# Kernel tuning notes

Measured on AMD Instinct MI355X. Metric: run time of the kernel, lower is better.

## Reference

```python
import jax, jax.numpy as jnp
import numpy as np

N, E, F_IN = 50000, 250000, 128
H1, H2, HEADS = 64, 32, 4
D1 = H1 * HEADS   # 256 = conv1 output dim (concat)
D2 = H2 * HEADS   # 128 = conv2 output dim (concat)
EPS_BN = 1e-5


def setup_inputs() -> dict:
    key = jax.random.key(0)
    ks = iter(jax.random.split(key, 64))
    def nrm(shape, scale=0.05):
        return jax.random.normal(next(ks), shape, dtype=jnp.float32) * scale
    inp = {}
    inp['x'] = jax.random.normal(next(ks), (N, F_IN), dtype=jnp.float32)
    inp['edge_index'] = jax.random.randint(next(ks), (2, E), 0, N, dtype=jnp.int32)
    inp['neg_edge_index'] = jax.random.randint(next(ks), (2, E), 0, N, dtype=jnp.int32)
    # conv1: TransformerConv(F_IN, 64, heads=4, beta=True, concat=True)
    inp['Wq1'] = nrm((F_IN, D1)); inp['bq1'] = jnp.zeros((D1,), jnp.float32)
    inp['Wk1'] = nrm((F_IN, D1)); inp['bk1'] = jnp.zeros((D1,), jnp.float32)
    inp['Wv1'] = nrm((F_IN, D1)); inp['bv1'] = jnp.zeros((D1,), jnp.float32)
    inp['Ws1'] = nrm((F_IN, D1)); inp['bs1'] = jnp.zeros((D1,), jnp.float32)
    inp['Wb1'] = nrm((3 * D1, 1))
    inp['g1'] = jnp.ones((D1,), jnp.float32); inp['be1'] = jnp.zeros((D1,), jnp.float32)
    inp['m1'] = nrm((D1,), 0.01); inp['v1'] = jax.random.uniform(next(ks), (D1,), dtype=jnp.float32) + 0.5
    # conv2: TransformerConv(256, 32, heads=4, beta=True, concat=True)
    inp['Wq2'] = nrm((D1, D2)); inp['bq2'] = jnp.zeros((D2,), jnp.float32)
    inp['Wk2'] = nrm((D1, D2)); inp['bk2'] = jnp.zeros((D2,), jnp.float32)
    inp['Wv2'] = nrm((D1, D2)); inp['bv2'] = jnp.zeros((D2,), jnp.float32)
    inp['Ws2'] = nrm((D1, D2)); inp['bs2'] = jnp.zeros((D2,), jnp.float32)
    inp['Wb2'] = nrm((3 * D2, 1))
    inp['g2'] = jnp.ones((D2,), jnp.float32); inp['be2'] = jnp.zeros((D2,), jnp.float32)
    inp['m2'] = nrm((D2,), 0.01); inp['v2'] = jax.random.uniform(next(ks), (D2,), dtype=jnp.float32) + 0.5
    # conv3: TransformerConv(128, 1, heads=1, beta=True, concat=False)
    inp['Wq3'] = nrm((D2, 1)); inp['bq3'] = jnp.zeros((1,), jnp.float32)
    inp['Wk3'] = nrm((D2, 1)); inp['bk3'] = jnp.zeros((1,), jnp.float32)
    inp['Wv3'] = nrm((D2, 1)); inp['bv3'] = jnp.zeros((1,), jnp.float32)
    inp['Ws3'] = nrm((D2, 1)); inp['bs3'] = jnp.zeros((1,), jnp.float32)
    inp['Wb3'] = nrm((3, 1))
    inp['c1'] = jnp.float32(0.5); inp['c2'] = jnp.float32(0.5)
    return inp


def _tconv(h, src, dst, Wq, bq, Wk, bk, Wv, bv, Ws, bs, Wb, heads, dh):
    # PyG TransformerConv with beta=True, root_weight=True. Messages flow src -> dst.
    n = h.shape[0]
    q = (h @ Wq + bq).reshape(n, heads, dh)
    k = (h @ Wk + bk).reshape(n, heads, dh)
    v = (h @ Wv + bv).reshape(n, heads, dh)
    score = jnp.einsum('ehd,ehd->eh', q[dst], k[src]) / jnp.sqrt(jnp.float32(dh))  # [E,H]
    m = jax.ops.segment_max(score, dst, num_segments=n)
    m = jnp.where(jnp.isfinite(m), m, jnp.float32(0.0))  # empty segments
    p = jnp.exp(score - m[dst])
    denom = jax.ops.segment_sum(p, dst, num_segments=n)
    alpha = p / (denom[dst] + 1e-16)
    out = jax.ops.segment_sum(alpha[:, :, None] * v[src], dst, num_segments=n)  # [N,H,dh]
    out = out.reshape(n, heads * dh)  # concat (heads=1 for conv3 -> same as mean)
    x_r = h @ Ws + bs
    beta = jax.nn.sigmoid(jnp.concatenate([out, x_r, out - x_r], axis=-1) @ Wb)  # [N,1]
    return beta * x_r + (1.0 - beta) * out


def _bn_eval(x, g, b, m, v):
    return (x - m) * jax.lax.rsqrt(v + EPS_BN) * g + b


def reference(x, edge_index, neg_edge_index,
              Wq1, bq1, Wk1, bk1, Wv1, bv1, Ws1, bs1, Wb1, g1, be1, m1, v1,
              Wq2, bq2, Wk2, bk2, Wv2, bv2, Ws2, bs2, Wb2, g2, be2, m2, v2,
              Wq3, bq3, Wk3, bk3, Wv3, bv3, Ws3, bs3, Wb3, c1, c2):
    src, dst = edge_index[0], edge_index[1]
    h = _tconv(x, src, dst, Wq1, bq1, Wk1, bk1, Wv1, bv1, Ws1, bs1, Wb1, HEADS, H1)
    h = jax.nn.elu(_bn_eval(h, g1, be1, m1, v1))
    h = _tconv(h, src, dst, Wq2, bq2, Wk2, bk2, Wv2, bv2, Ws2, bs2, Wb2, HEADS, H2)
    z = jax.nn.elu(_bn_eval(h, g2, be2, m2, v2))
    pos = -jnp.log(jax.nn.sigmoid(jnp.sum(z[src] * z[dst], axis=1)) + 1e-15).mean()
    ns, nd = neg_edge_index[0], neg_edge_index[1]
    neg = -jnp.log(1.0 - jax.nn.sigmoid(jnp.sum(z[ns] * z[nd], axis=1)) + 1e-15).mean()
    r_loss = pos + neg
    x_out = _tconv(z, src, dst, Wq3, bq3, Wk3, bk3, Wv3, bv3, Ws3, bs3, Wb3, 1, 1)
    return (x_out, r_loss, c1, c2)
```

## Files before the change

kernel.cpp:

```cpp
#include <hip/hip_runtime.h>
#include <hip/hip_bf16.h>

template<int BM, int BN, int BK>
__global__ __launch_bounds__(256) void sgemm_bias(
    const float* __restrict__ A, const float* __restrict__ W,
    const float* __restrict__ bias, float* __restrict__ C,
    int Nr, int K, int Dout)
{
  __shared__ float As[BK][BM];
  __shared__ float Ws[BK][BN];
  const int t  = threadIdx.x;
  const int tx = t & 15;
  const int ty = t >> 4;
  const int row0 = blockIdx.x * BM;
  const int col0 = blockIdx.y * BN;
  float acc[4][4] = {};
  for (int kb = 0; kb < K; kb += BK) {
    {
      int m  = t >> 2;
      int kq = (t & 3) * 8;
      int r  = row0 + m;
      float4 a0, a1;
      if (r < Nr) {
        const float* p = A + (long long)r * K + kb + kq;
        a0 = *(const float4*)p;
        a1 = *(const float4*)(p + 4);
      } else {
        a0 = make_float4(0.f,0.f,0.f,0.f); a1 = a0;
      }
      As[kq+0][m]=a0.x; As[kq+1][m]=a0.y; As[kq+2][m]=a0.z; As[kq+3][m]=a0.w;
      As[kq+4][m]=a1.x; As[kq+5][m]=a1.y; As[kq+6][m]=a1.z; As[kq+7][m]=a1.w;
    }
    {
      int cw = tx * 4;
#pragma unroll
      for (int it = 0; it < 2; ++it) {
        int kw = ty + it * 16;
        float4 w4 = *(const float4*)(W + (long long)(kb + kw) * Dout + col0 + cw);
        *(float4*)&Ws[kw][cw] = w4;
      }
    }
    __syncthreads();
#pragma unroll
    for (int kk = 0; kk < BK; ++kk) {
      float4 a4 = *(const float4*)&As[kk][ty * 4];
      float4 b4 = *(const float4*)&Ws[kk][tx * 4];
      float av[4] = {a4.x, a4.y, a4.z, a4.w};
      float bv[4] = {b4.x, b4.y, b4.z, b4.w};
#pragma unroll
      for (int i = 0; i < 4; ++i)
#pragma unroll
        for (int j = 0; j < 4; ++j)
          acc[i][j] += av[i] * bv[j];
    }
    __syncthreads();
  }
  float4 bb = *(const float4*)(bias + col0 + tx * 4);
  float bv4[4] = {bb.x, bb.y, bb.z, bb.w};
#pragma unroll
  for (int i = 0; i < 4; ++i) {
    int r = row0 + ty * 4 + i;
    if (r < Nr) {
      float4 o;
      o.x = acc[i][0] + bv4[0];
      o.y = acc[i][1] + bv4[1];
      o.z = acc[i][2] + bv4[2];
      o.w = acc[i][3] + bv4[3];
      *(float4*)(C + (long long)r * Dout + col0 + tx * 4) = o;
    }
  }
}

__global__ __launch_bounds__(256) void csr_hist(
    const int* __restrict__ ei, int E, int* __restrict__ cnt)
{
  int e = blockIdx.x * 256 + threadIdx.x;
  if (e >= E) return;
  atomicAdd(&cnt[ei[E + e]], 1);
}

__global__ __launch_bounds__(256) void csr_scan1(
    const int* __restrict__ cnt, int* __restrict__ excl,
    int* __restrict__ chunkSums, int N)
{
  int b = blockIdx.x, t = threadIdx.x;
  int lane = t & 63, w = t >> 6;
  int base = b * 1024 + t * 4;
  int c[4];
#pragma unroll
  for (int j = 0; j < 4; ++j) c[j] = (base + j < N) ? cnt[base + j] : 0;
  int ts = c[0] + c[1] + c[2] + c[3];
  int s = ts;
#pragma unroll
  for (int d = 1; d < 64; d <<= 1) {
    int u = __shfl_up(s, d, 64);
    if (lane >= d) s += u;
  }
  __shared__ int wsum[4];
  if (lane == 63) wsum[w] = s;
  __syncthreads();
  int woff = 0;
  for (int i = 0; i < w; ++i) woff += wsum[i];
  int off = woff + s - ts;
#pragma unroll
  for (int j = 0; j < 4; ++j) {
    if (base + j < N) excl[base + j] = off;
    off += c[j];
  }
  if (t == 0) chunkSums[b] = wsum[0] + wsum[1] + wsum[2] + wsum[3];
}

__global__ void csr_scan2(int* __restrict__ chunkSums, int nch,
                          int* __restrict__ rowptr, int N, int E)
{
  int lane = threadIdx.x;
  int v = (lane < nch) ? chunkSums[lane] : 0;
  int s = v;
#pragma unroll
  for (int d = 1; d < 64; d <<= 1) {
    int u = __shfl_up(s, d, 64);
    if (lane >= d) s += u;
  }
  if (lane < nch) chunkSums[lane] = s - v;
  if (lane == 0) rowptr[N] = E;
}

__global__ __launch_bounds__(256) void csr_scan3(
    int* __restrict__ rowptr, const int* __restrict__ chunkSums, int N)
{
  int i = blockIdx.x * 256 + threadIdx.x;
  if (i < N) rowptr[i] += chunkSums[i >> 10];
}

__global__ __launch_bounds__(256) void csr_scatter(
    const int* __restrict__ ei, int E, const int* __restrict__ rowptr,
    int* __restrict__ fill, int* __restrict__ csr_src)
{
  int e = blockIdx.x * 256 + threadIdx.x;
  if (e >= E) return;
  int s = ei[e], d = ei[E + e];
  int pos = atomicAdd(&fill[d], 1);
  csr_src[rowptr[d] + pos] = s;
}

template<int D, int H>
__global__ __launch_bounds__(256) void attn_fused(
    const int* __restrict__ rowptr, const int* __restrict__ csr_src,
    const float* __restrict__ q, const float* __restrict__ k,
    const float* __restrict__ v, float* __restrict__ o, int N)
{
  constexpr int PER = D / 64;
  constexpr int DH  = D / H;
  int node = blockIdx.x * 4 + (threadIdx.x >> 6);
  if (node >= N) return;
  int lane = threadIdx.x & 63;
  int j0   = lane * PER;
  const float inv = 1.0f / sqrtf((float)DH);

  float qv[PER];
  if constexpr (PER == 4) {
    float4 t4 = *(const float4*)(q + (long long)node * D + j0);
    qv[0]=t4.x; qv[1]=t4.y; qv[2]=t4.z; qv[3]=t4.w;
  } else {
    float2 t2 = *(const float2*)(q + (long long)node * D + j0);
    qv[0]=t2.x; qv[1]=t2.y;
  }

  float m = -INFINITY, den = 0.f;
  float acc[PER] = {};
  int beg = rowptr[node], end = rowptr[node + 1];
  for (int i = beg; i < end; ++i) {
    int s = csr_src[i];
    float kv[PER], vv[PER];
    if constexpr (PER == 4) {
      float4 t4 = *(const float4*)(k + (long long)s * D + j0);
      kv[0]=t4.x; kv[1]=t4.y; kv[2]=t4.z; kv[3]=t4.w;
      float4 u4 = *(const float4*)(v + (long long)s * D + j0);
      vv[0]=u4.x; vv[1]=u4.y; vv[2]=u4.z; vv[3]=u4.w;
    } else {
      float2 t2 = *(const float2*)(k + (long long)s * D + j0);
      kv[0]=t2.x; kv[1]=t2.y;
      float2 u2 = *(const float2*)(v + (long long)s * D + j0);
      vv[0]=u2.x; vv[1]=u2.y;
    }
    float dot = 0.f;
#pragma unroll
    for (int j = 0; j < PER; ++j) dot += qv[j] * kv[j];
    dot += __shfl_xor(dot, 8, 64);
    dot += __shfl_xor(dot, 4, 64);
    dot += __shfl_xor(dot, 2, 64);
    dot += __shfl_xor(dot, 1, 64);
    float score = dot * inv;
    float nm = fmaxf(m, score);
    float scale = __expf(m - nm);
    float p = __expf(score - nm);
    den = den * scale + p;
#pragma unroll
    for (int j = 0; j < PER; ++j) acc[j] = acc[j] * scale + p * vv[j];
    m = nm;
  }
  float r = 1.f / (den + 1e-16f);
  if constexpr (PER == 4) {
    float4 w4; w4.x = acc[0]*r; w4.y = acc[1]*r; w4.z = acc[2]*r; w4.w = acc[3]*r;
    *(float4*)(o + (long long)node * D + j0) = w4;
  } else {
    float2 w2; w2.x = acc[0]*r; w2.y = acc[1]*r;
    *(float2*)(o + (long long)node * D + j0) = w2;
  }
}

template<int D>
__global__ __launch_bounds__(256) void node_gate2(
    const float* __restrict__ o, const float* __restrict__ xr,
    const float* __restrict__ Wb, const float* __restrict__ g,
    const float* __restrict__ be, const float* __restrict__ bm,
    const float* __restrict__ bv, float* __restrict__ out, int N)
{
  constexpr int PER = D / 64;
  int node = blockIdx.x * 4 + (threadIdx.x >> 6);
  if (node >= N) return;
  int lane = threadIdx.x & 63;
  int j0   = lane * PER;
  float ov[PER], xv[PER];
  if constexpr (PER == 4) {
    float4 o4 = *(const float4*)(o  + (long long)node * D + j0);
    float4 x4 = *(const float4*)(xr + (long long)node * D + j0);
    ov[0]=o4.x; ov[1]=o4.y; ov[2]=o4.z; ov[3]=o4.w;
    xv[0]=x4.x; xv[1]=x4.y; xv[2]=x4.z; xv[3]=x4.w;
  } else {
    float2 o2 = *(const float2*)(o  + (long long)node * D + j0);
    float2 x2 = *(const float2*)(xr + (long long)node * D + j0);
    ov[0]=o2.x; ov[1]=o2.y;
    xv[0]=x2.x; xv[1]=x2.y;
  }
  float dot = 0.f;
#pragma unroll
  for (int i = 0; i < PER; ++i) {
    int j = j0 + i;
    dot += ov[i] * Wb[j] + xv[i] * Wb[D + j] + (ov[i] - xv[i]) * Wb[2 * D + j];
  }
#pragma unroll
  for (int off = 32; off >= 1; off >>= 1) dot += __shfl_xor(dot, off, 64);
  float beta = 1.f / (1.f + expf(-dot));
  float res[PER];
#pragma unroll
  for (int i = 0; i < PER; ++i) {
    int j = j0 + i;
    float h = beta * xv[i] + (1.f - beta) * ov[i];
    float y = (h - bm[j]) * rsqrtf(bv[j] + 1e-5f) * g[j] + be[j];
    res[i] = y > 0.f ? y : expf(y) - 1.f;
  }
  if constexpr (PER == 4) {
    float4 w; w.x=res[0]; w.y=res[1]; w.z=res[2]; w.w=res[3];
    *(float4*)(out + (long long)node * D + j0) = w;
  } else {
    float2 w; w.x=res[0]; w.y=res[1];
    *(float2*)(out + (long long)node * D + j0) = w;
  }
}

__global__ __launch_bounds__(256) void loss_kernel(
    const int* __restrict__ ei, const int* __restrict__ nei,
    const float* __restrict__ z, int E, float* __restrict__ acc)
{
  int lane = threadIdx.x & 63;
  int wib  = threadIdx.x >> 6;
  int sub  = lane >> 5, r = lane & 31;
  long long gw = ((long long)blockIdx.x * blockDim.x + threadIdx.x) >> 6;
  long long nw = ((long long)gridDim.x * blockDim.x) >> 6;
  float lpos = 0.f, lneg = 0.f;
  for (long long w = gw * 2 + sub; w < 2LL * E; w += nw * 2) {
    int isneg = (w >= E);
    const int* ep = isneg ? nei : ei;
    long long idx = isneg ? w - E : w;
    int s = ep[idx], d = ep[E + idx];
    float4 a = *(const float4*)(z + (long long)s * 128 + r * 4);
    float4 b = *(const float4*)(z + (long long)d * 128 + r * 4);
    float dot = a.x * b.x + a.y * b.y + a.z * b.z + a.w * b.w;
#pragma unroll
    for (int off = 16; off >= 1; off >>= 1) dot += __shfl_xor(dot, off, 64);
    if (r == 0) {
      float sg = 1.f / (1.f + expf(-dot));
      if (isneg) lneg += -logf(1.f - sg + 1e-15f);
      else       lpos += -logf(sg + 1e-15f);
    }
  }
#pragma unroll
  for (int off = 32; off >= 1; off >>= 1) {
    lpos += __shfl_xor(lpos, off, 64);
    lneg += __shfl_xor(lneg, off, 64);
  }
  __shared__ float sp[4], sn[4];
  if (lane == 0) { sp[wib] = lpos; sn[wib] = lneg; }
  __syncthreads();
  if (threadIdx.x == 0) {
    float P = 0.f, Ng = 0.f;
    for (int i = 0; i < 4; ++i) { P += sp[i]; Ng += sn[i]; }
    atomicAdd(acc, P);
    atomicAdd(acc + 1, Ng);
  }
}

__global__ __launch_bounds__(256) void gemv4(
    const float* __restrict__ z,
    const float* __restrict__ Wq, const float* __restrict__ bq,
    const float* __restrict__ Wk, const float* __restrict__ bk,
    const float* __restrict__ Wv, const float* __restrict__ bv,
    const float* __restrict__ Ws, const float* __restrict__ bs,
    float* __restrict__ q3, float* __restrict__ k3,
    float* __restrict__ v3, float* __restrict__ s3, int N)
{
  int node = blockIdx.x * 4 + (threadIdx.x >> 6);
  if (node >= N) return;
  int lane = threadIdx.x & 63;
  float2 zv = *(const float2*)(z + (long long)node * 128 + lane * 2);
  float aq = zv.x * Wq[lane*2] + zv.y * Wq[lane*2+1];
  float ak = zv.x * Wk[lane*2] + zv.y * Wk[lane*2+1];
  float av = zv.x * Wv[lane*2] + zv.y * Wv[lane*2+1];
  float as_ = zv.x * Ws[lane*2] + zv.y * Ws[lane*2+1];
#pragma unroll
  for (int off = 32; off >= 1; off >>= 1) {
    aq  += __shfl_xor(aq,  off, 64);
    ak  += __shfl_xor(ak,  off, 64);
    av  += __shfl_xor(av,  off, 64);
    as_ += __shfl_xor(as_, off, 64);
  }
  if (lane == 0) {
    q3[node] = aq + bq[0];
    k3[node] = ak + bk[0];
    v3[node] = av + bv[0];
    s3[node] = as_ + bs[0];
  }
}

__global__ __launch_bounds__(256) void attn3_node(
    const int* __restrict__ rowptr, const int* __restrict__ csr_src,
    const float* __restrict__ q3, const float* __restrict__ k3,
    const float* __restrict__ v3, const float* __restrict__ s3,
    const float* __restrict__ Wb3, float* __restrict__ out, int N)
{
  int n = blockIdx.x * 256 + threadIdx.x;
  if (n >= N) return;
  float qd = q3[n];
  float m = -INFINITY, den = 0.f, acc = 0.f;
  int beg = rowptr[n], end = rowptr[n + 1];
  for (int i = beg; i < end; ++i) {
    int s = csr_src[i];
    float sc = qd * k3[s];
    float nm = fmaxf(m, sc);
    float scale = __expf(m - nm);
    float p = __expf(sc - nm);
    den = den * scale + p;
    acc = acc * scale + p * v3[s];
    m = nm;
  }
  float on = acc / (den + 1e-16f);
  float xr = s3[n];
  float tv = on * Wb3[0] + xr * Wb3[1] + (on - xr) * Wb3[2];
  float b = 1.f / (1.f + expf(-tv));
  out[n] = b * xr + (1.f - b) * on;
}

__global__ void finalize_kernel(const float* __restrict__ acc,
                                const float* __restrict__ c1, const float* __restrict__ c2,
                                float* __restrict__ out, int N, int E)
{
  out[N]     = acc[0] / (float)E + acc[1] / (float)E;
  out[N + 1] = c1[0];
  out[N + 2] = c2[0];
}

extern "C" void kernel_launch(void* const* d_in, const int* in_sizes, int n_in,
                              void* d_out, int out_size, void* d_ws, size_t ws_size,
                              hipStream_t stream)
{
  const float* x   = (const float*)d_in[0];
  const int*   ei  = (const int*)d_in[1];
  const int*   nei = (const int*)d_in[2];
  const float* Wq1 = (const float*)d_in[3];  const float* bq1 = (const float*)d_in[4];
  const float* Wk1 = (const float*)d_in[5];  const float* bk1 = (const float*)d_in[6];
  const float* Wv1 = (const float*)d_in[7];  const float* bv1 = (const float*)d_in[8];
  const float* Ws1 = (const float*)d_in[9];  const float* bs1 = (const float*)d_in[10];
  const float* Wb1 = (const float*)d_in[11];
  const float* g1  = (const float*)d_in[12]; const float* be1 = (const float*)d_in[13];
  const float* m1  = (const float*)d_in[14]; const float* v1  = (const float*)d_in[15];
  const float* Wq2 = (const float*)d_in[16]; const float* bq2 = (const float*)d_in[17];
  const float* Wk2 = (const float*)d_in[18]; const float* bk2 = (const float*)d_in[19];
  const float* Wv2 = (const float*)d_in[20]; const float* bv2 = (const float*)d_in[21];
  const float* Ws2 = (const float*)d_in[22]; const float* bs2 = (const float*)d_in[23];
  const float* Wb2 = (const float*)d_in[24];
  const float* g2  = (const float*)d_in[25]; const float* be2 = (const float*)d_in[26];
  const float* m2  = (const float*)d_in[27]; const float* v2  = (const float*)d_in[28];
  const float* Wq3 = (const float*)d_in[29]; const float* bq3 = (const float*)d_in[30];
  const float* Wk3 = (const float*)d_in[31]; const float* bk3 = (const float*)d_in[32];
  const float* Wv3 = (const float*)d_in[33]; const float* bv3 = (const float*)d_in[34];
  const float* Ws3 = (const float*)d_in[35]; const float* bs3 = (const float*)d_in[36];
  const float* Wb3 = (const float*)d_in[37];
  const float* c1  = (const float*)d_in[38]; const float* c2  = (const float*)d_in[39];

  const int N = in_sizes[0] / 128;
  const int E = in_sizes[1] / 2;

  float* ws = (float*)d_ws;
  float* B0 = ws;
  float* B1 = B0 + (size_t)N * 256;
  float* B2 = B1 + (size_t)N * 256;
  int* rowptr = (int*)(B2 + (size_t)N * 256);
  int* cnt    = rowptr + (N + 1);
  int* csrs   = cnt + N;
  int* chks   = csrs + E;
  float* accbuf = (float*)(chks + 64);

  size_t need = ((size_t)3 * N * 256) * 4 + ((size_t)2 * N + 1 + E + 64) * 4 + 8;
  if (ws_size < need) return;

  float* out = (float*)d_out;
  dim3 blk(256);
  dim3 gemm1g((N + 63) / 64, 256 / 64);
  dim3 gemm2g((N + 63) / 64, 128 / 64);
  int ng  = (N + 3) / 4;
  int egE = (E + 255) / 256;
  int egN = (N + 255) / 256;
  int nch = (N + 1023) / 1024;

  (void)hipMemsetAsync(cnt, 0, (size_t)N * sizeof(int), stream);
  csr_hist<<<egE, blk, 0, stream>>>(ei, E, cnt);
  csr_scan1<<<nch, blk, 0, stream>>>(cnt, rowptr, chks, N);
  csr_scan2<<<1, 64, 0, stream>>>(chks, nch, rowptr, N, E);
  csr_scan3<<<egN, blk, 0, stream>>>(rowptr, chks, N);
  (void)hipMemsetAsync(cnt, 0, (size_t)N * sizeof(int), stream);
  csr_scatter<<<egE, blk, 0, stream>>>(ei, E, rowptr, cnt, csrs);

  sgemm_bias<64,64,32><<<gemm1g, blk, 0, stream>>>(x, Wq1, bq1, B0, N, 128, 256);
  sgemm_bias<64,64,32><<<gemm1g, blk, 0, stream>>>(x, Wk1, bk1, B1, N, 128, 256);
  sgemm_bias<64,64,32><<<gemm1g, blk, 0, stream>>>(x, Wv1, bv1, B2, N, 128, 256);
  attn_fused<256,4><<<ng, blk, 0, stream>>>(rowptr, csrs, B0, B1, B2, B0, N);
  sgemm_bias<64,64,32><<<gemm1g, blk, 0, stream>>>(x, Ws1, bs1, B1, N, 128, 256);
  node_gate2<256><<<ng, blk, 0, stream>>>(B0, B1, Wb1, g1, be1, m1, v1, B2, N);

  float* q2p = B0;
  float* k2p = B0 + (size_t)N * 128;
  float* v2p = B1;
  float* s2p = B1 + (size_t)N * 128;
  sgemm_bias<64,64,32><<<gemm2g, blk, 0, stream>>>(B2, Wq2, bq2, q2p, N, 256, 128);
  sgemm_bias<64,64,32><<<gemm2g, blk, 0, stream>>>(B2, Wk2, bk2, k2p, N, 256, 128);
  sgemm_bias<64,64,32><<<gemm2g, blk, 0, stream>>>(B2, Wv2, bv2, v2p, N, 256, 128);
  attn_fused<128,4><<<ng, blk, 0, stream>>>(rowptr, csrs, q2p, k2p, v2p, q2p, N);
  sgemm_bias<64,64,32><<<gemm2g, blk, 0, stream>>>(B2, Ws2, bs2, s2p, N, 256, 128);
  float* z = k2p;
  node_gate2<128><<<ng, blk, 0, stream>>>(q2p, s2p, Wb2, g2, be2, m2, v2, z, N);

  (void)hipMemsetAsync(accbuf, 0, 2 * sizeof(float), stream);
  loss_kernel<<<1024, blk, 0, stream>>>(ei, nei, z, E, accbuf);

  float* q3 = B1;
  float* k3 = B1 + (size_t)N;
  float* v3 = B1 + (size_t)2 * N;
  float* s3 = B1 + (size_t)3 * N;
  gemv4<<<ng, blk, 0, stream>>>(z, Wq3, bq3, Wk3, bk3, Wv3, bv3, Ws3, bs3, q3, k3, v3, s3, N);
  attn3_node<<<egN, blk, 0, stream>>>(rowptr, csrs, q3, k3, v3, s3, Wb3, out, N);

  finalize_kernel<<<1, 1, 0, stream>>>(accbuf, c1, c2, out, N, E);
}
```

Measured before the change: 893.4 us.

## Replace FP32 SIMT GEMMs with FP16 MFMA GEMMs using pretransposed weights

Swaps the shared-memory FP32 tiled SGEMM for a wavefront-level MFMA 16x16x32 f16 kernel. Activations are converted to half in registers and read directly from global memory, with no LDS staging. Weights are transposed and converted to FP16 by a new prep kernel on each call. This aims to cut the projection GEMM cost by using the matrix cores, at the price of reduced input precision and uncoalesced, non-vectorized output stores.

```diff
diff --git a/kernel.cpp b/kernel.cpp
--- a/kernel.cpp
+++ b/kernel.cpp
@@ -1,72 +1,78 @@
 #include <hip/hip_runtime.h>
 #include <hip/hip_bf16.h>
 
-template<int BM, int BN, int BK>
-__global__ __launch_bounds__(256) void sgemm_bias(
-    const float* __restrict__ A, const float* __restrict__ W,
-    const float* __restrict__ bias, float* __restrict__ C,
-    int Nr, int K, int Dout)
-{
-  __shared__ float As[BK][BM];
-  __shared__ float Ws[BK][BN];
-  const int t  = threadIdx.x;
-  const int tx = t & 15;
-  const int ty = t >> 4;
-  const int row0 = blockIdx.x * BM;
-  const int col0 = blockIdx.y * BN;
-  float acc[4][4] = {};
-  for (int kb = 0; kb < K; kb += BK) {
-    {
-      int m  = t >> 2;
-      int kq = (t & 3) * 8;
-      int r  = row0 + m;
-      float4 a0, a1;
-      if (r < Nr) {
-        const float* p = A + (long long)r * K + kb + kq;
-        a0 = *(const float4*)p;
-        a1 = *(const float4*)(p + 4);
+typedef _Float16 half8 __attribute__((ext_vector_type(8)));
+typedef float f32x4 __attribute__((ext_vector_type(4)));
+
+__global__ __launch_bounds__(256) void prep_w(
+    const float* __restrict__ W0, const float* __restrict__ W1,
+    const float* __restrict__ W2, const float* __restrict__ W3,
+    _Float16* __restrict__ T, int K, int D)
+{
+  int idx = blockIdx.x * 256 + threadIdx.x;
+  int tot = K * D;
+  if (idx >= 4 * tot) return;
+  int which = idx / tot, rem = idx - which * tot;
+  int d = rem / K, k = rem - d * K;
+  const float* W = which == 0 ? W0 : which == 1 ? W1 : which == 2 ? W2 : W3;
+  T[idx] = (_Float16)W[(long long)k * D + d];
+}
+
+template<int K>
+__global__ __launch_bounds__(256) void mfma_gemm(
+    const float* __restrict__ A, const _Float16* __restrict__ Wt,
+    const float* __restrict__ bias, float* __restrict__ C, int Nr, int Dout)
+{
+  int lane = threadIdx.x & 63;
+  int w    = threadIdx.x >> 6;
+  int wm = w >> 1, wn = w & 1;
+  int row0 = blockIdx.x * 64 + wm * 32;
+  int col0 = blockIdx.y * 64 + wn * 32;
+  int lr = lane & 15;
+  int lk = (lane >> 4) * 8;
+
+  f32x4 acc[2][2] = {};
+#pragma unroll
+  for (int kb = 0; kb < K; kb += 32) {
+    half8 a[2], b[2];
+#pragma unroll
+    for (int mt = 0; mt < 2; ++mt) {
+      int row = row0 + mt * 16 + lr;
+      if (row < Nr) {
+        const float* p = A + (long long)row * K + kb + lk;
+        float4 f0 = *(const float4*)p;
+        float4 f1 = *(const float4*)(p + 4);
+        a[mt][0] = (_Float16)f0.x; a[mt][1] = (_Float16)f0.y;
+        a[mt][2] = (_Float16)f0.z; a[mt][3] = (_Float16)f0.w;
+        a[mt][4] = (_Float16)f1.x; a[mt][5] = (_Float16)f1.y;
+        a[mt][6] = (_Float16)f1.z; a[mt][7] = (_Float16)f1.w;
       } else {
-        a0 = make_float4(0.f,0.f,0.f,0.f); a1 = a0;
-      }
-      As[kq+0][m]=a0.x; As[kq+1][m]=a0.y; As[kq+2][m]=a0.z; As[kq+3][m]=a0.w;
-      As[kq+4][m]=a1.x; As[kq+5][m]=a1.y; As[kq+6][m]=a1.z; As[kq+7][m]=a1.w;
-    }
-    {
-      int cw = tx * 4;
-#pragma unroll
-      for (int it = 0; it < 2; ++it) {
-        int kw = ty + it * 16;
-        float4 w4 = *(const float4*)(W + (long long)(kb + kw) * Dout + col0 + cw);
-        *(float4*)&Ws[kw][cw] = w4;
+        a[mt] = half8{};
       }
     }
-    __syncthreads();
-#pragma unroll
-    for (int kk = 0; kk < BK; ++kk) {
-      float4 a4 = *(const float4*)&As[kk][ty * 4];
-      float4 b4 = *(const float4*)&Ws[kk][tx * 4];
-      float av[4] = {a4.x, a4.y, a4.z, a4.w};
-      float bv[4] = {b4.x, b4.y, b4.z, b4.w};
-#pragma unroll
-      for (int i = 0; i < 4; ++i)
-#pragma unroll
-        for (int j = 0; j < 4; ++j)
-          acc[i][j] += av[i] * bv[j];
+#pragma unroll
+    for (int nt = 0; nt < 2; ++nt) {
+      int col = col0 + nt * 16 + lr;
+      b[nt] = *(const half8*)(Wt + (long long)col * K + kb + lk);
     }
-    __syncthreads();
-  }
-  float4 bb = *(const float4*)(bias + col0 + tx * 4);
-  float bv4[4] = {bb.x, bb.y, bb.z, bb.w};
-#pragma unroll
-  for (int i = 0; i < 4; ++i) {
-    int r = row0 + ty * 4 + i;
-    if (r < Nr) {
-      float4 o;
-      o.x = acc[i][0] + bv4[0];
-      o.y = acc[i][1] + bv4[1];
-      o.z = acc[i][2] + bv4[2];
-      o.w = acc[i][3] + bv4[3];
-      *(float4*)(C + (long long)r * Dout + col0 + tx * 4) = o;
+#pragma unroll
+    for (int mt = 0; mt < 2; ++mt)
+#pragma unroll
+      for (int nt = 0; nt < 2; ++nt)
+        acc[mt][nt] = __builtin_amdgcn_mfma_f32_16x16x32_f16(a[mt], b[nt], acc[mt][nt], 0, 0, 0);
+  }
+#pragma unroll
+  for (int nt = 0; nt < 2; ++nt) {
+    int col = col0 + nt * 16 + lr;
+    float bc = bias[col];
+#pragma unroll
+    for (int mt = 0; mt < 2; ++mt) {
+      int r0 = row0 + mt * 16 + (lane >> 4) * 4;
+#pragma unroll
+      for (int i = 0; i < 4; ++i) {
+        int row = r0 + i;
+        if (row < Nr) C[(long long)row * Dout + col] = acc[mt][nt][i] + bc;
+      }
     }
   }
 }
@@ -410,18 +416,25 @@
   int* csrs   = cnt + N;
   int* chks   = csrs + E;
   float* accbuf = (float*)(chks + 64);
-
-  size_t need = ((size_t)3 * N * 256) * 4 + ((size_t)2 * N + 1 + E + 64) * 4 + 8;
+  uintptr_t wp = ((uintptr_t)(accbuf + 2) + 63) & ~(uintptr_t)63;
+  _Float16* wt1 = (_Float16*)wp;
+  _Float16* wt2 = wt1 + 4 * 32768;
+
+  size_t need = ((size_t)3 * N * 256) * 4 + ((size_t)2 * N + 1 + E + 64) * 4 + 8
+              + 64 + 8 * 32768 * sizeof(_Float16);
   if (ws_size < need) return;
 
   float* out = (float*)d_out;
   dim3 blk(256);
-  dim3 gemm1g((N + 63) / 64, 256 / 64);
-  dim3 gemm2g((N + 63) / 64, 128 / 64);
   int ng  = (N + 3) / 4;
   int egE = (E + 255) / 256;
   int egN = (N + 255) / 256;
   int nch = (N + 1023) / 1024;
+  dim3 g1grid((N + 63) / 64, 256 / 64);
+  dim3 g2grid((N + 63) / 64, 128 / 64);
+
+  prep_w<<<(4 * 32768 + 255) / 256, blk, 0, stream>>>(Wq1, Wk1, Wv1, Ws1, wt1, 128, 256);
+  prep_w<<<(4 * 32768 + 255) / 256, blk, 0, stream>>>(Wq2, Wk2, Wv2, Ws2, wt2, 256, 128);
 
   (void)hipMemsetAsync(cnt, 0, (size_t)N * sizeof(int), stream);
   csr_hist<<<egE, blk, 0, stream>>>(ei, E, cnt);
@@ -431,22 +444,22 @@
   (void)hipMemsetAsync(cnt, 0, (size_t)N * sizeof(int), stream);
   csr_scatter<<<egE, blk, 0, stream>>>(ei, E, rowptr, cnt, csrs);
 
-  sgemm_bias<64,64,32><<<gemm1g, blk, 0, stream>>>(x, Wq1, bq1, B0, N, 128, 256);
-  sgemm_bias<64,64,32><<<gemm1g, blk, 0, stream>>>(x, Wk1, bk1, B1, N, 128, 256);
-  sgemm_bias<64,64,32><<<gemm1g, blk, 0, stream>>>(x, Wv1, bv1, B2, N, 128, 256);
+  mfma_gemm<128><<<g1grid, blk, 0, stream>>>(x, wt1 + 0 * 32768, bq1, B0, N, 256);
+  mfma_gemm<128><<<g1grid, blk, 0, stream>>>(x, wt1 + 1 * 32768, bk1, B1, N, 256);
+  mfma_gemm<128><<<g1grid, blk, 0, stream>>>(x, wt1 + 2 * 32768, bv1, B2, N, 256);
   attn_fused<256,4><<<ng, blk, 0, stream>>>(rowptr, csrs, B0, B1, B2, B0, N);
-  sgemm_bias<64,64,32><<<gemm1g, blk, 0, stream>>>(x, Ws1, bs1, B1, N, 128, 256);
+  mfma_gemm<128><<<g1grid, blk, 0, stream>>>(x, wt1 + 3 * 32768, bs1, B1, N, 256);
   node_gate2<256><<<ng, blk, 0, stream>>>(B0, B1, Wb1, g1, be1, m1, v1, B2, N);
 
   float* q2p = B0;
   float* k2p = B0 + (size_t)N * 128;
   float* v2p = B1;
   float* s2p = B1 + (size_t)N * 128;
-  sgemm_bias<64,64,32><<<gemm2g, blk, 0, stream>>>(B2, Wq2, bq2, q2p, N, 256, 128);
-  sgemm_bias<64,64,32><<<gemm2g, blk, 0, stream>>>(B2, Wk2, bk2, k2p, N, 256, 128);
-  sgemm_bias<64,64,32><<<gemm2g, blk, 0, stream>>>(B2, Wv2, bv2, v2p, N, 256, 128);
+  mfma_gemm<256><<<g2grid, blk, 0, stream>>>(B2, wt2 + 0 * 32768, bq2, q2p, N, 128);
+  mfma_gemm<256><<<g2grid, blk, 0, stream>>>(B2, wt2 + 1 * 32768, bk2, k2p, N, 128);
+  mfma_gemm<256><<<g2grid, blk, 0, stream>>>(B2, wt2 + 2 * 32768, bv2, v2p, N, 128);
   attn_fused<128,4><<<ng, blk, 0, stream>>>(rowptr, csrs, q2p, k2p, v2p, q2p, N);
-  sgemm_bias<64,64,32><<<gemm2g, blk, 0, stream>>>(B2, Ws2, bs2, s2p, N, 256, 128);
+  mfma_gemm<256><<<g2grid, blk, 0, stream>>>(B2, wt2 + 3 * 32768, bs2, s2p, N, 128);
   float* z = k2p;
   node_gate2<128><<<ng, blk, 0, stream>>>(q2p, s2p, Wb2, g2, be2, m2, v2, z, N);
 
```

New measurement: 852.3 us. 1.05x faster.
